# Performance work log

Measured on AMD Instinct MI355X. Metric: run time of the kernel, lower is better.

Reference implementation:

```python
import jax, jax.numpy as jnp
import numpy as np

ALPHA = 300.0   # attractor_alpha
N_ATT = 16      # n_attractors
MIN_D = 0.001
MAX_D = 10.0


def _resize_bilinear_ac(x, out_h, out_w):
    """Bilinear resize with align_corners=True on trailing (H, W) dims of [B,C,h,w]."""
    h, w = x.shape[-2], x.shape[-1]
    ys = jnp.arange(out_h, dtype=jnp.float32) * ((h - 1) / max(out_h - 1, 1))
    xs = jnp.arange(out_w, dtype=jnp.float32) * ((w - 1) / max(out_w - 1, 1))
    y0 = jnp.floor(ys).astype(jnp.int32); y1 = jnp.minimum(y0 + 1, h - 1)
    x0 = jnp.floor(xs).astype(jnp.int32); x1 = jnp.minimum(x0 + 1, w - 1)
    wy = (ys - y0.astype(jnp.float32))[:, None]   # [out_h, 1]
    wx = (xs - x0.astype(jnp.float32))[None, :]   # [1, out_w]
    v00 = x[..., y0[:, None], x0[None, :]]
    v01 = x[..., y0[:, None], x1[None, :]]
    v10 = x[..., y1[:, None], x0[None, :]]
    v11 = x[..., y1[:, None], x1[None, :]]
    top = v00 * (1 - wx) + v01 * wx
    bot = v10 * (1 - wx) + v11 * wx
    return top * (1 - wy) + bot * wy


def setup_inputs() -> dict:
    key = jax.random.key(0)
    k = jax.random.split(key, 7)
    B, C, H, W = 4, 128, 192, 192
    n_bins = 64
    x = jax.random.normal(k[0], (B, C, H, W), dtype=jnp.float32)
    prev_bin = jax.random.uniform(k[1], (B, n_bins, H // 2, W // 2), dtype=jnp.float32)
    prev_bin_embedding = jax.random.normal(k[2], (B, C, H // 2, W // 2), dtype=jnp.float32)
    w1 = jax.random.normal(k[3], (128, 128), dtype=jnp.float32) * 0.05
    b1 = jnp.zeros((128,), dtype=jnp.float32)
    w2 = jax.random.normal(k[4], (2 * N_ATT, 128), dtype=jnp.float32) * 0.05
    b2 = jnp.zeros((2 * N_ATT,), dtype=jnp.float32)
    return {"x": x, "prev_bin": prev_bin, "prev_bin_embedding": prev_bin_embedding,
            "w1": w1, "b1": b1, "w2": w2, "b2": b2}


def reference(x, prev_bin, prev_bin_embedding, w1, b1, w2, b2):
    B, C, H, W = x.shape
    # add (interpolated) previous bin embedding
    pe = _resize_bilinear_ac(prev_bin_embedding, H, W)
    h = x + pe
    # per-pixel MLP (two 1x1 convs)
    h = jax.nn.relu(jnp.einsum('bchw,oc->bohw', h, w1) + b1[:, None, None])
    att = jax.nn.relu(jnp.einsum('bchw,oc->bohw', h, w2) + b2[:, None, None]) + 0.001
    # [B, n_attractors, 2, H, W] -> take normed attractor points
    att = att.reshape(B, N_ATT, 2, H, W)[:, :, 0]          # [B, nA, H, W]
    # upsample previous bin centers to feature resolution
    bc = _resize_bilinear_ac(prev_bin, H, W)               # [B, nB, H, W]
    # broadcast-subtract + inverse attractor + mean over attractors
    dx = att[:, :, None, :, :] - bc[:, None, :, :, :]      # [B, nA, nB, H, W]
    delta_c = jnp.mean(dx / (1.0 + ALPHA * dx * dx), axis=1)  # gamma = 2
    bin_new_centers = bc + delta_c
    bin_centers = (MAX_D - MIN_D) * bin_new_centers + MIN_D
    bin_centers = jnp.clip(jnp.sort(bin_centers, axis=1), MIN_D, MAX_D)
    return bin_new_centers, bin_centers
```

## Files before the change

### kernel.cpp

```cpp
#include <hip/hip_runtime.h>

constexpr int Bc = 4, Cc = 128, Hc = 192, Wc = 192;
constexpr int HI = 96, WI = 96;
constexpr int NB = 64;
constexpr int NA = 16;
constexpr float SCL = 95.0f / 191.0f;

typedef __attribute__((ext_vector_type(8))) short bf16x8;
typedef __attribute__((ext_vector_type(4))) float f32x4;

__device__ __forceinline__ unsigned short f2bf(float f) {
  unsigned u = __builtin_bit_cast(unsigned, f);
  unsigned r = (u + 0x7FFFu + ((u >> 16) & 1u)) >> 16;
  return (unsigned short)r;
}
__device__ __forceinline__ float rcp_fast(float r) {
#if defined(__has_builtin)
#if __has_builtin(__builtin_amdgcn_rcpf)
  return __builtin_amdgcn_rcpf(r);
#else
  return 1.0f / r;
#endif
#else
  return 1.0f / r;
#endif
}

__global__ __launch_bounds__(256) void k_prep(
    const float* __restrict__ w1, const float* __restrict__ w2,
    unsigned short* __restrict__ w1bf, unsigned short* __restrict__ w2bf)
{
  const int t = blockIdx.x * 256 + threadIdx.x;
  if (t < 16384) {
    w1bf[t] = f2bf(w1[t]);
  } else {
    const int u = t - 16384;
    const int j = u >> 7, c = u & 127;
    w2bf[u] = f2bf(w2[(2 * j) * 128 + c]);
  }
}

__global__ __launch_bounds__(256, 4) void k_att(
    const float* __restrict__ x, const float* __restrict__ pbe,
    const unsigned short* __restrict__ w1bf, const float* __restrict__ b1,
    const unsigned short* __restrict__ w2bf, const float* __restrict__ b2,
    float* __restrict__ att)
{
  constexpr int PH = 136;
  constexpr int RP = 37;
  __shared__ __align__(16) unsigned char smem[128 * RP * 4];
  float*          row_s = (float*)smem;
  unsigned short* a1_s  = (unsigned short*)smem;

  const int tid = threadIdx.x;
  const int xg0 = blockIdx.x * 64;
  const int y = blockIdx.y;
  const int b = blockIdx.z;

  const float ysf = y * SCL;
  const int y0 = (int)ysf;
  const int y1 = min(y0 + 1, HI - 1);
  const float wy = ysf - (float)y0;
  const int xi0 = (int)(xg0 * SCL);

  const int lane = tid & 63;
  const int wv = tid >> 6;
  const int ln = lane & 15;
  const int qd = lane >> 4;
  const int m0 = wv * 16;

  const int px = m0 + ln;
  const int xg = xg0 + px;
  const float xsf = (float)xg * SCL;
  const int x0i = (int)xsf;
  const float wx = xsf - (float)x0i;
  const int xl = x0i - xi0;

  float xr[32];
  #pragma unroll
  for (int kt = 0; kt < 4; ++kt) {
    #pragma unroll
    for (int j = 0; j < 8; ++j) {
      const int c = kt * 32 + qd * 8 + j;
      xr[kt * 8 + j] = x[((size_t)(b * Cc + c) * Hc + y) * Wc + xg];
    }
  }

  #pragma unroll
  for (int i = 0; i < 18; ++i) {
    const int f = tid + 256 * i;
    const int c = f / 36;
    const int xi = f - c * 36;
    const int xgl = min(xi0 + xi, WI - 1);
    const float* p = pbe + (size_t)(b * Cc + c) * (HI * WI);
    const float top = p[y0 * WI + xgl];
    const float bot = p[y1 * WI + xgl];
    row_s[c * RP + xi] = top + wy * (bot - top);
  }
  __syncthreads();

  bf16x8 af[4];
  #pragma unroll
  for (int kt = 0; kt < 4; ++kt) {
    #pragma unroll
    for (int j = 0; j < 8; ++j) {
      const int c = kt * 32 + qd * 8 + j;
      const float v0 = row_s[c * RP + xl];
      const float v1 = row_s[c * RP + xl + 1];
      af[kt][j] = (short)f2bf(xr[kt * 8 + j] + v0 + wx * (v1 - v0));
    }
  }
  __syncthreads();

  f32x4 acc[8];
  #pragma unroll
  for (int nt = 0; nt < 8; ++nt) acc[nt] = f32x4{0.f, 0.f, 0.f, 0.f};
  #pragma unroll
  for (int nt = 0; nt < 8; ++nt) {
    #pragma unroll
    for (int kt = 0; kt < 4; ++kt) {
      const bf16x8 bf = *(const bf16x8*)&w1bf[(nt * 16 + ln) * 128 + kt * 32 + qd * 8];
      acc[nt] = __builtin_amdgcn_mfma_f32_16x16x32_bf16(af[kt], bf, acc[nt], 0, 0, 0);
    }
  }

  #pragma unroll
  for (int nt = 0; nt < 8; ++nt) {
    const int n = nt * 16 + ln;
    const float bias = b1[n];
    #pragma unroll
    for (int r = 0; r < 4; ++r) {
      const int m = m0 + qd * 4 + r;
      a1_s[m * PH + n] = f2bf(fmaxf(acc[nt][r] + bias, 0.f));
    }
  }

  f32x4 acc2 = f32x4{0.f, 0.f, 0.f, 0.f};
  #pragma unroll
  for (int kt = 0; kt < 4; ++kt) {
    const bf16x8 a2 = *(const bf16x8*)&a1_s[(m0 + ln) * PH + kt * 32 + qd * 8];
    const bf16x8 b2f = *(const bf16x8*)&w2bf[ln * 128 + kt * 32 + qd * 8];
    acc2 = __builtin_amdgcn_mfma_f32_16x16x32_bf16(a2, b2f, acc2, 0, 0, 0);
  }
  const float bias2 = b2[2 * ln];
  #pragma unroll
  for (int r = 0; r < 4; ++r) {
    const int opx = m0 + qd * 4 + r;
    const float v = fmaxf(acc2[r] + bias2, 0.f) + 0.001f;
    att[((size_t)((b * Hc + y) * Wc) + xg0 + opx) * NA + ln] = v;
  }
}

__global__ __launch_bounds__(192, 2) void k_bins(
    const float* __restrict__ pb, const float* __restrict__ att,
    float* __restrict__ out0, float* __restrict__ out1)
{
  __shared__ __align__(16) float row_s[NB][WI];

  const int tid = threadIdx.x;
  const int y = blockIdx.x;
  const int b = blockIdx.y;

  const float ysf = y * SCL;
  const int y0 = (int)ysf;
  const int y1 = min(y0 + 1, HI - 1);
  const float wy = ysf - (float)y0;

  float am[16];
  {
    const float4* ap = (const float4*)(att + ((size_t)((b * Hc + y) * Wc) + tid) * NA);
    const float4 a0 = ap[0], a1 = ap[1], a2 = ap[2], a3 = ap[3];
    am[0] = a0.x;  am[1] = a0.y;  am[2] = a0.z;  am[3] = a0.w;
    am[4] = a1.x;  am[5] = a1.y;  am[6] = a1.z;  am[7] = a1.w;
    am[8] = a2.x;  am[9] = a2.y;  am[10] = a2.z; am[11] = a2.w;
    am[12] = a3.x; am[13] = a3.y; am[14] = a3.z; am[15] = a3.w;
  }

  #pragma unroll
  for (int i = 0; i < 8; ++i) {
    const int u = tid + 192 * i;
    const int k = u / 24;
    const int g = u - k * 24;
    const float* base = pb + (size_t)(b * NB + k) * (HI * WI);
    const float4 t4 = *(const float4*)&base[y0 * WI + g * 4];
    const float4 b4 = *(const float4*)&base[y1 * WI + g * 4];
    float4 r;
    r.x = t4.x + wy * (b4.x - t4.x);
    r.y = t4.y + wy * (b4.y - t4.y);
    r.z = t4.z + wy * (b4.z - t4.z);
    r.w = t4.w + wy * (b4.w - t4.w);
    *(float4*)&row_s[k][g * 4] = r;
  }
  __syncthreads();

  const float xsf = tid * SCL;
  const int x0 = (int)xsf;
  const float wx = xsf - (float)x0;

  const size_t obase = (size_t)(b * NB) * (Hc * Wc) + (size_t)y * Wc + tid;
  float v[NB];

  #pragma unroll
  for (int kb = 0; kb < NB; kb += 4) {
    float bc[4], dl[4];
    #pragma unroll
    for (int q = 0; q < 4; ++q) {
      const int k = kb + q;
      const float v0 = row_s[k][x0], v1 = row_s[k][x0 + 1];
      bc[q] = v0 + wx * (v1 - v0);
      dl[q] = 0.f;
    }
    #pragma unroll
    for (int j = 0; j < NA; ++j) {
      const float a = am[j];
      #pragma unroll
      for (int q = 0; q < 4; ++q) {
        const float d = a - bc[q];
        const float rq = fmaf(300.f * d, d, 1.f);
        dl[q] = fmaf(d, rcp_fast(rq), dl[q]);
      }
    }
    #pragma unroll
    for (int q = 0; q < 4; ++q) {
      const float bnc = fmaf(dl[q], 1.f / 16.f, bc[q]);
      out0[obase + (size_t)(kb + q) * (Hc * Wc)] = bnc;
      v[kb + q] = fmaf(9.999f, bnc, 0.001f);
    }
  }

  #pragma unroll
  for (int size = 2; size <= NB; size <<= 1) {
    #pragma unroll
    for (int stride = size >> 1; stride >= 1; stride >>= 1) {
      #pragma unroll
      for (int i = 0; i < NB; ++i) {
        if ((i & stride) == 0) {
          const int j = i | stride;
          const bool asc = ((i & size) == 0);
          const float a = v[i], c = v[j];
          const float lo = fminf(a, c), hi = fmaxf(a, c);
          v[i] = asc ? lo : hi;
          v[j] = asc ? hi : lo;
        }
      }
    }
  }

  #pragma unroll
  for (int k = 0; k < NB; ++k) {
    out1[obase + (size_t)k * (Hc * Wc)] = fminf(fmaxf(v[k], 0.001f), 10.0f);
  }
}

extern "C" void kernel_launch(void* const* d_in, const int* in_sizes, int n_in,
                              void* d_out, int out_size, void* d_ws, size_t ws_size,
                              hipStream_t stream) {
  const float* x   = (const float*)d_in[0];
  const float* pb  = (const float*)d_in[1];
  const float* pbe = (const float*)d_in[2];
  const float* w1  = (const float*)d_in[3];
  const float* b1  = (const float*)d_in[4];
  const float* w2  = (const float*)d_in[5];
  const float* b2  = (const float*)d_in[6];

  float* out0 = (float*)d_out;
  float* out1 = out0 + (size_t)Bc * NB * Hc * Wc;

  unsigned short* w1bf = (unsigned short*)d_ws;
  unsigned short* w2bf = w1bf + 16384;
  float* att = (float*)((char*)d_ws + 65536);

  k_prep<<<72, 256, 0, stream>>>(w1, w2, w1bf, w2bf);

  dim3 g1(Wc / 64, Hc, Bc);
  k_att<<<g1, 256, 0, stream>>>(x, pbe, w1bf, b1, w2bf, b2, att);

  dim3 g2(Hc, Bc);
  k_bins<<<g2, 192, 0, stream>>>(pb, att, out0, out1);
}
```

Baseline: 238.0 us.

## Store attractors as bf16, batch global loads ahead of use, raise k_bins occupancy

The intermediate attractor tensor is now written and read in bf16 instead of fp32, which halves its traffic between the two kernels. In both kernels the global loads for the prev_bin and embedding rows are issued into registers before any interpolation math, so more memory requests are in flight at once. k_bins launch bounds go from 2 to 3 blocks per SM. The costs are lower precision on the attractor values, which may shift the outputs slightly, and higher register pressure from the staged loads.

```diff
diff --git a/kernel.cpp b/kernel.cpp
--- a/kernel.cpp
+++ b/kernel.cpp
@@ -13,6 +13,10 @@
   unsigned u = __builtin_bit_cast(unsigned, f);
   unsigned r = (u + 0x7FFFu + ((u >> 16) & 1u)) >> 16;
   return (unsigned short)r;
+}
+__device__ __forceinline__ float bf2f(unsigned short h) {
+  unsigned u = ((unsigned)h) << 16;
+  return __builtin_bit_cast(float, u);
 }
 __device__ __forceinline__ float rcp_fast(float r) {
 #if defined(__has_builtin)
@@ -44,7 +48,7 @@
     const float* __restrict__ x, const float* __restrict__ pbe,
     const unsigned short* __restrict__ w1bf, const float* __restrict__ b1,
     const unsigned short* __restrict__ w2bf, const float* __restrict__ b2,
-    float* __restrict__ att)
+    unsigned short* __restrict__ att16)
 {
   constexpr int PH = 136;
   constexpr int RP = 37;
@@ -76,16 +80,7 @@
   const float wx = xsf - (float)x0i;
   const int xl = x0i - xi0;
 
-  float xr[32];
-  #pragma unroll
-  for (int kt = 0; kt < 4; ++kt) {
-    #pragma unroll
-    for (int j = 0; j < 8; ++j) {
-      const int c = kt * 32 + qd * 8 + j;
-      xr[kt * 8 + j] = x[((size_t)(b * Cc + c) * Hc + y) * Wc + xg];
-    }
-  }
-
+  float tops[18], bots[18];
   #pragma unroll
   for (int i = 0; i < 18; ++i) {
     const int f = tid + 256 * i;
@@ -93,9 +88,25 @@
     const int xi = f - c * 36;
     const int xgl = min(xi0 + xi, WI - 1);
     const float* p = pbe + (size_t)(b * Cc + c) * (HI * WI);
-    const float top = p[y0 * WI + xgl];
-    const float bot = p[y1 * WI + xgl];
-    row_s[c * RP + xi] = top + wy * (bot - top);
+    tops[i] = p[y0 * WI + xgl];
+    bots[i] = p[y1 * WI + xgl];
+  }
+  float xr[32];
+  #pragma unroll
+  for (int kt = 0; kt < 4; ++kt) {
+    #pragma unroll
+    for (int j = 0; j < 8; ++j) {
+      const int c = kt * 32 + qd * 8 + j;
+      xr[kt * 8 + j] = x[((size_t)(b * Cc + c) * Hc + y) * Wc + xg];
+    }
+  }
+
+  #pragma unroll
+  for (int i = 0; i < 18; ++i) {
+    const int f = tid + 256 * i;
+    const int c = f / 36;
+    const int xi = f - c * 36;
+    row_s[c * RP + xi] = tops[i] + wy * (bots[i] - tops[i]);
   }
   __syncthreads();
 
@@ -147,12 +158,12 @@
   for (int r = 0; r < 4; ++r) {
     const int opx = m0 + qd * 4 + r;
     const float v = fmaxf(acc2[r] + bias2, 0.f) + 0.001f;
-    att[((size_t)((b * Hc + y) * Wc) + xg0 + opx) * NA + ln] = v;
-  }
-}
-
-__global__ __launch_bounds__(192, 2) void k_bins(
-    const float* __restrict__ pb, const float* __restrict__ att,
+    att16[((size_t)((b * Hc + y) * Wc) + xg0 + opx) * NA + ln] = f2bf(v);
+  }
+}
+
+__global__ __launch_bounds__(192, 3) void k_bins(
+    const float* __restrict__ pb, const unsigned short* __restrict__ att16,
     float* __restrict__ out0, float* __restrict__ out1)
 {
   __shared__ __align__(16) float row_s[NB][WI];
@@ -166,29 +177,40 @@
   const int y1 = min(y0 + 1, HI - 1);
   const float wy = ysf - (float)y0;
 
-  float am[16];
+  bf16x8 a16a, a16b;
   {
-    const float4* ap = (const float4*)(att + ((size_t)((b * Hc + y) * Wc) + tid) * NA);
-    const float4 a0 = ap[0], a1 = ap[1], a2 = ap[2], a3 = ap[3];
-    am[0] = a0.x;  am[1] = a0.y;  am[2] = a0.z;  am[3] = a0.w;
-    am[4] = a1.x;  am[5] = a1.y;  am[6] = a1.z;  am[7] = a1.w;
-    am[8] = a2.x;  am[9] = a2.y;  am[10] = a2.z; am[11] = a2.w;
-    am[12] = a3.x; am[13] = a3.y; am[14] = a3.z; am[15] = a3.w;
-  }
-
+    const bf16x8* ap = (const bf16x8*)(att16 + ((size_t)((b * Hc + y) * Wc) + tid) * NA);
+    a16a = ap[0];
+    a16b = ap[1];
+  }
+  float4 t4a[8], b4a[8];
   #pragma unroll
   for (int i = 0; i < 8; ++i) {
     const int u = tid + 192 * i;
     const int k = u / 24;
     const int g = u - k * 24;
     const float* base = pb + (size_t)(b * NB + k) * (HI * WI);
-    const float4 t4 = *(const float4*)&base[y0 * WI + g * 4];
-    const float4 b4 = *(const float4*)&base[y1 * WI + g * 4];
+    t4a[i] = *(const float4*)&base[y0 * WI + g * 4];
+    b4a[i] = *(const float4*)&base[y1 * WI + g * 4];
+  }
+
+  float am[16];
+  #pragma unroll
+  for (int j = 0; j < 8; ++j) {
+    am[j]     = bf2f((unsigned short)a16a[j]);
+    am[8 + j] = bf2f((unsigned short)a16b[j]);
+  }
+
+  #pragma unroll
+  for (int i = 0; i < 8; ++i) {
+    const int u = tid + 192 * i;
+    const int k = u / 24;
+    const int g = u - k * 24;
     float4 r;
-    r.x = t4.x + wy * (b4.x - t4.x);
-    r.y = t4.y + wy * (b4.y - t4.y);
-    r.z = t4.z + wy * (b4.z - t4.z);
-    r.w = t4.w + wy * (b4.w - t4.w);
+    r.x = t4a[i].x + wy * (b4a[i].x - t4a[i].x);
+    r.y = t4a[i].y + wy * (b4a[i].y - t4a[i].y);
+    r.z = t4a[i].z + wy * (b4a[i].z - t4a[i].z);
+    r.w = t4a[i].w + wy * (b4a[i].w - t4a[i].w);
     *(float4*)&row_s[k][g * 4] = r;
   }
   __syncthreads();
@@ -268,13 +290,13 @@
 
   unsigned short* w1bf = (unsigned short*)d_ws;
   unsigned short* w2bf = w1bf + 16384;
-  float* att = (float*)((char*)d_ws + 65536);
+  unsigned short* att16 = (unsigned short*)((char*)d_ws + 65536);
 
   k_prep<<<72, 256, 0, stream>>>(w1, w2, w1bf, w2bf);
 
   dim3 g1(Wc / 64, Hc, Bc);
-  k_att<<<g1, 256, 0, stream>>>(x, pbe, w1bf, b1, w2bf, b2, att);
+  k_att<<<g1, 256, 0, stream>>>(x, pbe, w1bf, b1, w2bf, b2, att16);
 
   dim3 g2(Hc, Bc);
-  k_bins<<<g2, 192, 0, stream>>>(pb, att, out0, out1);
-}
+  k_bins<<<g2, 192, 0, stream>>>(pb, att16, out0, out1);
+}
```

Measured after the change: 240.4 us. Within noise of the previous version (+1.0%).
